# Optimization experiments

Measured on AMD Instinct MI355X. Metric: run time of the kernel, lower is better.

Reference implementation:

```python
import jax, jax.numpy as jnp
import numpy as np

HIDDEN = 1024
HEADS = 16
HEAD_DIM = HIDDEN // HEADS


def setup_inputs() -> dict:
    key = jax.random.key(0)
    kx, kq, kk, kv, ko = jax.random.split(key, 5)
    s = 1.0 / np.sqrt(HIDDEN)
    return {
        "x": jax.random.normal(kx, (2, 2048, HIDDEN), dtype=jnp.float32),
        # nn.Linear weights, stored [out, in] like torch
        "Wq": jax.random.uniform(kq, (HIDDEN, HIDDEN), jnp.float32, -s, s),
        "Wk": jax.random.uniform(kk, (HIDDEN, HIDDEN), jnp.float32, -s, s),
        "Wv": jax.random.uniform(kv, (HIDDEN, HIDDEN), jnp.float32, -s, s),
        "Wo": jax.random.uniform(ko, (HIDDEN, HIDDEN), jnp.float32, -s, s),
    }


def reference(x, Wq, Wk, Wv, Wo):
    B, S, D = x.shape
    H, Hd = HEADS, HEAD_DIM

    def proj(W):  # torch Linear: x @ W.T -> [B,H,S,Hd]
        return (x @ W.T).reshape(B, S, H, Hd).transpose(0, 2, 1, 3)

    q, k, v = proj(Wq), proj(Wk), proj(Wv)
    scores = jnp.einsum("bhsd,bhtd->bhst", q, k) / max(Hd ** 0.5, 1e-6)
    causal = jnp.tril(jnp.ones((S, S), dtype=bool))  # True = keep
    scores = jnp.where(causal, scores, -jnp.inf)
    attn = jax.nn.softmax(scores, axis=-1)
    y = jnp.einsum("bhst,bhtd->bhsd", attn, v)
    y = y.transpose(0, 2, 1, 3).reshape(B, S, D)
    return y @ Wo.T
```

## Files before the change

kernel.cpp:

```cpp
#include <hip/hip_runtime.h>
#include <hip/hip_bf16.h>


#define S_LEN  2048
#define BATCH  2
#define DMODEL 1024
#define NHEADS 16
#define HDIM   64
#define QKV_LD 3072

typedef short short8 __attribute__((ext_vector_type(8)));
typedef float f32x4  __attribute__((ext_vector_type(4)));

__device__ __forceinline__ float b2f(unsigned short u) {
    union { unsigned int i; float f; } x; x.i = ((unsigned int)u) << 16; return x.f;
}
__device__ __forceinline__ unsigned short f2b(float f) {
    union { float f; unsigned int i; } x; x.f = f;
    unsigned int r = x.i + 0x7fffu + ((x.i >> 16) & 1u);
    return (unsigned short)(r >> 16);
}

__device__ __forceinline__ void gload16(const unsigned short* g, unsigned short* l) {
    __builtin_amdgcn_global_load_lds(
        (const __attribute__((address_space(1))) unsigned int*)g,
        (__attribute__((address_space(3))) unsigned int*)l, 16, 0, 0);
}

__device__ __forceinline__ unsigned short* swzp(unsigned short* base, int row, int col) {
    int byte = (col << 1) ^ ((((row >> 3) ^ row) & 7) << 4);
    return base + (row << 6) + (byte >> 1);
}

__global__ void cast_kernel(const float* __restrict__ in, unsigned short* __restrict__ out, int n4) {
    int i = blockIdx.x * blockDim.x + threadIdx.x;
    if (i >= n4) return;
    float4 v = ((const float4*)in)[i];
    unsigned int lo = (unsigned int)f2b(v.x) | ((unsigned int)f2b(v.y) << 16);
    unsigned int hi = (unsigned int)f2b(v.z) | ((unsigned int)f2b(v.w) << 16);
    ((uint2*)out)[i] = make_uint2(lo, hi);
}

__global__ void cast_w4(const float* __restrict__ w0, const float* __restrict__ w1,
                        const float* __restrict__ w2, const float* __restrict__ w3,
                        unsigned short* __restrict__ out) {
    int i = blockIdx.x * blockDim.x + threadIdx.x;
    if (i >= (1 << 20)) return;
    int seg = i >> 18;
    const float* src = seg == 0 ? w0 : seg == 1 ? w1 : seg == 2 ? w2 : w3;
    float4 v = ((const float4*)src)[i & 0x3FFFF];
    unsigned int lo = (unsigned int)f2b(v.x) | ((unsigned int)f2b(v.y) << 16);
    unsigned int hi = (unsigned int)f2b(v.z) | ((unsigned int)f2b(v.w) << 16);
    ((uint2*)out)[i] = make_uint2(lo, hi);
}

template<int OUT_BF16>
__global__ __launch_bounds__(256) void gemm128(const unsigned short* __restrict__ A,
                                               const unsigned short* __restrict__ W,
                                               unsigned short* __restrict__ Cb,
                                               float* __restrict__ Cf,
                                               int N, int K) {
    __shared__ unsigned short As[128 * 64];
    __shared__ unsigned short Bs[128 * 64];
    const int tid  = threadIdx.x;
    const int lane = tid & 63;
    const int wave = tid >> 6;
    const int bm = blockIdx.y * 128;
    const int bn = blockIdx.x * 128;
    const int wr = (wave >> 1) * 64;
    const int wc = (wave & 1) * 64;
    const int l15 = lane & 15;
    const int l4  = lane >> 4;

    const int srow = wave * 32 + (lane >> 3);
    const int scol = (lane & 7) * 8;
    const unsigned short* Ag = A + (size_t)(bm + srow) * K + scol;
    const unsigned short* Wg = W + (size_t)(bn + srow) * K + scol;
    unsigned short* Al = As + wave * 32 * 64;
    unsigned short* Bl = Bs + wave * 32 * 64;

    f32x4 acc[4][4];
#pragma unroll
    for (int i = 0; i < 4; ++i)
#pragma unroll
        for (int j = 0; j < 4; ++j) acc[i][j] = (f32x4){0.f, 0.f, 0.f, 0.f};

    for (int k0 = 0; k0 < K; k0 += 64) {
        __syncthreads();
#pragma unroll
        for (int i = 0; i < 4; ++i) {
            gload16(Ag + k0 + (size_t)(i * 8) * K, Al + i * 8 * 64);
            gload16(Wg + k0 + (size_t)(i * 8) * K, Bl + i * 8 * 64);
        }
        __syncthreads();
#pragma unroll
        for (int kk = 0; kk < 2; ++kk) {
            short8 af[4], bf[4];
#pragma unroll
            for (int mi = 0; mi < 4; ++mi)
                af[mi] = *(const short8*)&As[(wr + mi * 16 + l15) * 64 + kk * 32 + l4 * 8];
#pragma unroll
            for (int ni = 0; ni < 4; ++ni)
                bf[ni] = *(const short8*)&Bs[(wc + ni * 16 + l15) * 64 + kk * 32 + l4 * 8];
#pragma unroll
            for (int mi = 0; mi < 4; ++mi)
#pragma unroll
                for (int ni = 0; ni < 4; ++ni)
                    acc[mi][ni] = __builtin_amdgcn_mfma_f32_16x16x32_bf16(af[mi], bf[ni], acc[mi][ni], 0, 0, 0);
        }
    }
#pragma unroll
    for (int mi = 0; mi < 4; ++mi)
#pragma unroll
        for (int ni = 0; ni < 4; ++ni)
#pragma unroll
            for (int i = 0; i < 4; ++i) {
                int row = bm + wr + mi * 16 + l4 * 4 + i;
                int col = bn + wc + ni * 16 + l15;
                float v = acc[mi][ni][i];
                if constexpr (OUT_BF16) Cb[(size_t)row * N + col] = f2b(v);
                else                    Cf[(size_t)row * N + col] = v;
            }
}

__global__ __launch_bounds__(256) void attn_mfma(const unsigned short* __restrict__ Qp,
                                                 const unsigned short* __restrict__ Kp,
                                                 const unsigned short* __restrict__ Vp,
                                                 unsigned short* __restrict__ Yp) {
    __shared__ unsigned short Ks[64 * 64];
    __shared__ unsigned short Vt[64 * 64];
    __shared__ unsigned short Pl[4 * 16 * 64];
    const int tid  = threadIdx.x;
    const int lane = tid & 63;
    const int wq   = tid >> 6;
    const int l15  = lane & 15;
    const int l4   = lane >> 4;
    const int r    = tid >> 2;
    const int c4   = tid & 3;
    const int h = blockIdx.y, b = blockIdx.z;
    unsigned short* Pw = Pl + wq * (16 * 64);

#pragma unroll 1
    for (int qp = 0; qp < 2; ++qp) {
        const int qt = qp ? (31 - (int)blockIdx.x) : (int)blockIdx.x;
        short8 qf0, qf1;
        {
            const unsigned short* qb = Qp + ((size_t)(b * S_LEN + qt * 64 + wq * 16 + l15)) * QKV_LD
                                          + h * HDIM + l4 * 8;
            qf0 = *(const short8*)qb;
            qf1 = *(const short8*)(qb + 32);
        }
        f32x4 oacc[4];
        float mrow[4], lrow[4];
#pragma unroll
        for (int t = 0; t < 4; ++t) oacc[t] = (f32x4){0.f, 0.f, 0.f, 0.f};
#pragma unroll
        for (int i = 0; i < 4; ++i) { mrow[i] = -1e30f; lrow[i] = 0.f; }

#pragma unroll 1
        for (int kt = 0; kt <= qt; ++kt) {
            __syncthreads();
            {
                const size_t gb = ((size_t)(b * S_LEN + kt * 64 + r)) * QKV_LD + h * HDIM + c4 * 16;
                uint4 k0 = *(const uint4*)(Kp + gb);
                uint4 k1 = *(const uint4*)(Kp + gb + 8);
                uint4 v0 = *(const uint4*)(Vp + gb);
                uint4 v1 = *(const uint4*)(Vp + gb + 8);
                *(uint4*)swzp(Ks, r, c4 * 16)     = k0;
                *(uint4*)swzp(Ks, r, c4 * 16 + 8) = k1;
                const unsigned short* vs = (const unsigned short*)&v0;
#pragma unroll
                for (int j = 0; j < 8; ++j) *swzp(Vt, c4 * 16 + j, r) = vs[j];
                vs = (const unsigned short*)&v1;
#pragma unroll
                for (int j = 0; j < 8; ++j) *swzp(Vt, c4 * 16 + 8 + j, r) = vs[j];
            }
            __syncthreads();

            f32x4 sc[4];
#pragma unroll
            for (int t = 0; t < 4; ++t) sc[t] = (f32x4){0.f, 0.f, 0.f, 0.f};
#pragma unroll
            for (int t = 0; t < 4; ++t) {
                short8 kf = *(const short8*)swzp(Ks, t * 16 + l15, l4 * 8);
                sc[t] = __builtin_amdgcn_mfma_f32_16x16x32_bf16(qf0, kf, sc[t], 0, 0, 0);
            }
#pragma unroll
            for (int t = 0; t < 4; ++t) {
                short8 kf = *(const short8*)swzp(Ks, t * 16 + l15, 32 + l4 * 8);
                sc[t] = __builtin_amdgcn_mfma_f32_16x16x32_bf16(qf1, kf, sc[t], 0, 0, 0);
            }
            const bool diag = (kt == qt);
#pragma unroll
            for (int t = 0; t < 4; ++t)
#pragma unroll
                for (int i = 0; i < 4; ++i) {
                    float s = sc[t][i] * 0.125f;
                    if (diag && (t * 16 + l15 > wq * 16 + l4 * 4 + i)) s = -1e30f;
                    sc[t][i] = s;
                }
#pragma unroll
            for (int i = 0; i < 4; ++i) {
                float mx = fmaxf(fmaxf(sc[0][i], sc[1][i]), fmaxf(sc[2][i], sc[3][i]));
                mx = fmaxf(mx, __shfl_xor(mx, 1));
                mx = fmaxf(mx, __shfl_xor(mx, 2));
                mx = fmaxf(mx, __shfl_xor(mx, 4));
                mx = fmaxf(mx, __shfl_xor(mx, 8));
                const float mn = fmaxf(mrow[i], mx);
                const float al = __expf(mrow[i] - mn);
                mrow[i] = mn;
                float ls = 0.f;
#pragma unroll
                for (int t = 0; t < 4; ++t) {
                    float p = __expf(sc[t][i] - mn);
                    sc[t][i] = p;
                    ls += p;
                }
                ls += __shfl_xor(ls, 1);
                ls += __shfl_xor(ls, 2);
                ls += __shfl_xor(ls, 4);
                ls += __shfl_xor(ls, 8);
                lrow[i] = lrow[i] * al + ls;
#pragma unroll
                for (int t = 0; t < 4; ++t) oacc[t][i] *= al;
            }
#pragma unroll
            for (int t = 0; t < 4; ++t)
#pragma unroll
                for (int i = 0; i < 4; ++i)
                    *swzp(Pw, l4 * 4 + i, t * 16 + l15) = f2b(sc[t][i]);

            short8 pf0 = *(const short8*)swzp(Pw, l15, l4 * 8);
            short8 pf1 = *(const short8*)swzp(Pw, l15, 32 + l4 * 8);
#pragma unroll
            for (int td = 0; td < 4; ++td) {
                short8 vf = *(const short8*)swzp(Vt, td * 16 + l15, l4 * 8);
                oacc[td] = __builtin_amdgcn_mfma_f32_16x16x32_bf16(pf0, vf, oacc[td], 0, 0, 0);
            }
#pragma unroll
            for (int td = 0; td < 4; ++td) {
                short8 vf = *(const short8*)swzp(Vt, td * 16 + l15, 32 + l4 * 8);
                oacc[td] = __builtin_amdgcn_mfma_f32_16x16x32_bf16(pf1, vf, oacc[td], 0, 0, 0);
            }
        }
        float linv[4];
#pragma unroll
        for (int i = 0; i < 4; ++i) linv[i] = 1.0f / lrow[i];
        unsigned short* yb = Yp + ((size_t)(b * S_LEN + qt * 64 + wq * 16 + l4 * 4)) * DMODEL
                                + h * HDIM + l15;
#pragma unroll
        for (int i = 0; i < 4; ++i)
#pragma unroll
            for (int td = 0; td < 4; ++td)
                yb[(size_t)i * DMODEL + td * 16] = f2b(oacc[td][i] * linv[i]);
    }
}

extern "C" void kernel_launch(void* const* d_in, const int* in_sizes, int n_in,
                              void* d_out, int out_size, void* d_ws, size_t ws_size,
                              hipStream_t stream) {
    (void)in_sizes; (void)n_in; (void)out_size; (void)ws_size;
    const float* x  = (const float*)d_in[0];
    const float* Wq = (const float*)d_in[1];
    const float* Wk = (const float*)d_in[2];
    const float* Wv = (const float*)d_in[3];
    const float* Wo = (const float*)d_in[4];
    float* out = (float*)d_out;

    const size_t nx = (size_t)BATCH * S_LEN * DMODEL;
    const size_t nw = (size_t)DMODEL * DMODEL;
    char* ws = (char*)d_ws;
    unsigned short* xb    = (unsigned short*)ws; ws += nx * 2;
    unsigned short* wqkvb = (unsigned short*)ws; ws += nw * 3 * 2;
    unsigned short* wob   = (unsigned short*)ws; ws += nw * 2;
    unsigned short* qkv   = (unsigned short*)ws; ws += nx * 3 * 2;
    unsigned short* yb    = (unsigned short*)ws; ws += nx * 2;

    cast_kernel<<<(int)(nx / 4 + 255) / 256, 256, 0, stream>>>(x, xb, (int)(nx / 4));
    cast_w4<<<(1 << 20) / 256, 256, 0, stream>>>(Wq, Wk, Wv, Wo, wqkvb);

    dim3 gq(QKV_LD / 128, (BATCH * S_LEN) / 128);
    gemm128<1><<<gq, 256, 0, stream>>>(xb, wqkvb, qkv, nullptr, QKV_LD, DMODEL);

    dim3 ga(S_LEN / 128, NHEADS, BATCH);
    attn_mfma<<<ga, 256, 0, stream>>>(qkv, qkv + DMODEL, qkv + 2 * DMODEL, yb);

    dim3 go(DMODEL / 128, (BATCH * S_LEN) / 128);
    gemm128<0><<<go, 256, 0, stream>>>(yb, wob, nullptr, out, DMODEL, DMODEL);
}
```

Measured before the change: 241.2 us.

## Double-buffer K/V tiles with register prefetch and fold softmax scale into QKV GEMM

The attention loop now stages K/V tiles through two LDS buffers and prefetches the next tile's global loads into registers while the current tile is computed. This leaves one barrier per iteration instead of two and hides global load latency. The 1/sqrt(d) scale moves into the QKV projection epilogue, applied to the Q columns before the bf16 store, so the per-score multiply disappears. The cost is doubled K/V shared memory and extra live registers, which may reduce occupancy, plus a slight change in where bf16 rounding happens.

```diff
diff --git a/kernel.cpp b/kernel.cpp
--- a/kernel.cpp
+++ b/kernel.cpp
@@ -118,8 +118,12 @@
                 int row = bm + wr + mi * 16 + l4 * 4 + i;
                 int col = bn + wc + ni * 16 + l15;
                 float v = acc[mi][ni][i];
-                if constexpr (OUT_BF16) Cb[(size_t)row * N + col] = f2b(v);
-                else                    Cf[(size_t)row * N + col] = v;
+                if constexpr (OUT_BF16) {
+                    if (col < DMODEL) v *= 0.125f;
+                    Cb[(size_t)row * N + col] = f2b(v);
+                } else {
+                    Cf[(size_t)row * N + col] = v;
+                }
             }
 }
 
@@ -127,8 +131,8 @@
                                                  const unsigned short* __restrict__ Kp,
                                                  const unsigned short* __restrict__ Vp,
                                                  unsigned short* __restrict__ Yp) {
-    __shared__ unsigned short Ks[64 * 64];
-    __shared__ unsigned short Vt[64 * 64];
+    __shared__ unsigned short Ks[2][64 * 64];
+    __shared__ unsigned short Vt[2][64 * 64];
     __shared__ unsigned short Pl[4 * 16 * 64];
     const int tid  = threadIdx.x;
     const int lane = tid & 63;
@@ -157,37 +161,51 @@
 #pragma unroll
         for (int i = 0; i < 4; ++i) { mrow[i] = -1e30f; lrow[i] = 0.f; }
 
+        uint4 rk0, rk1, rv0, rv1;
+        {
+            const size_t gb = ((size_t)(b * S_LEN + r)) * QKV_LD + h * HDIM + c4 * 16;
+            rk0 = *(const uint4*)(Kp + gb);
+            rk1 = *(const uint4*)(Kp + gb + 8);
+            rv0 = *(const uint4*)(Vp + gb);
+            rv1 = *(const uint4*)(Vp + gb + 8);
+        }
+
 #pragma unroll 1
         for (int kt = 0; kt <= qt; ++kt) {
+            const int cur = kt & 1;
+            unsigned short* Kc = (unsigned short*)Ks[cur];
+            unsigned short* Vc = (unsigned short*)Vt[cur];
+            *(uint4*)swzp(Kc, r, c4 * 16)     = rk0;
+            *(uint4*)swzp(Kc, r, c4 * 16 + 8) = rk1;
+            {
+                const unsigned short* vs = (const unsigned short*)&rv0;
+#pragma unroll
+                for (int j = 0; j < 8; ++j) *swzp(Vc, c4 * 16 + j, r) = vs[j];
+                vs = (const unsigned short*)&rv1;
+#pragma unroll
+                for (int j = 0; j < 8; ++j) *swzp(Vc, c4 * 16 + 8 + j, r) = vs[j];
+            }
+            if (kt < qt) {
+                const size_t gb = ((size_t)(b * S_LEN + (kt + 1) * 64 + r)) * QKV_LD
+                                  + h * HDIM + c4 * 16;
+                rk0 = *(const uint4*)(Kp + gb);
+                rk1 = *(const uint4*)(Kp + gb + 8);
+                rv0 = *(const uint4*)(Vp + gb);
+                rv1 = *(const uint4*)(Vp + gb + 8);
+            }
             __syncthreads();
-            {
-                const size_t gb = ((size_t)(b * S_LEN + kt * 64 + r)) * QKV_LD + h * HDIM + c4 * 16;
-                uint4 k0 = *(const uint4*)(Kp + gb);
-                uint4 k1 = *(const uint4*)(Kp + gb + 8);
-                uint4 v0 = *(const uint4*)(Vp + gb);
-                uint4 v1 = *(const uint4*)(Vp + gb + 8);
-                *(uint4*)swzp(Ks, r, c4 * 16)     = k0;
-                *(uint4*)swzp(Ks, r, c4 * 16 + 8) = k1;
-                const unsigned short* vs = (const unsigned short*)&v0;
-#pragma unroll
-                for (int j = 0; j < 8; ++j) *swzp(Vt, c4 * 16 + j, r) = vs[j];
-                vs = (const unsigned short*)&v1;
-#pragma unroll
-                for (int j = 0; j < 8; ++j) *swzp(Vt, c4 * 16 + 8 + j, r) = vs[j];
-            }
-            __syncthreads();
 
             f32x4 sc[4];
 #pragma unroll
             for (int t = 0; t < 4; ++t) sc[t] = (f32x4){0.f, 0.f, 0.f, 0.f};
 #pragma unroll
             for (int t = 0; t < 4; ++t) {
-                short8 kf = *(const short8*)swzp(Ks, t * 16 + l15, l4 * 8);
+                short8 kf = *(const short8*)swzp(Kc, t * 16 + l15, l4 * 8);
                 sc[t] = __builtin_amdgcn_mfma_f32_16x16x32_bf16(qf0, kf, sc[t], 0, 0, 0);
             }
 #pragma unroll
             for (int t = 0; t < 4; ++t) {
-                short8 kf = *(const short8*)swzp(Ks, t * 16 + l15, 32 + l4 * 8);
+                short8 kf = *(const short8*)swzp(Kc, t * 16 + l15, 32 + l4 * 8);
                 sc[t] = __builtin_amdgcn_mfma_f32_16x16x32_bf16(qf1, kf, sc[t], 0, 0, 0);
             }
             const bool diag = (kt == qt);
@@ -195,7 +213,7 @@
             for (int t = 0; t < 4; ++t)
 #pragma unroll
                 for (int i = 0; i < 4; ++i) {
-                    float s = sc[t][i] * 0.125f;
+                    float s = sc[t][i];
                     if (diag && (t * 16 + l15 > wq * 16 + l4 * 4 + i)) s = -1e30f;
                     sc[t][i] = s;
                 }
@@ -234,15 +252,17 @@
             short8 pf1 = *(const short8*)swzp(Pw, l15, 32 + l4 * 8);
 #pragma unroll
             for (int td = 0; td < 4; ++td) {
-                short8 vf = *(const short8*)swzp(Vt, td * 16 + l15, l4 * 8);
+                short8 vf = *(const short8*)swzp(Vc, td * 16 + l15, l4 * 8);
                 oacc[td] = __builtin_amdgcn_mfma_f32_16x16x32_bf16(pf0, vf, oacc[td], 0, 0, 0);
             }
 #pragma unroll
             for (int td = 0; td < 4; ++td) {
-                short8 vf = *(const short8*)swzp(Vt, td * 16 + l15, 32 + l4 * 8);
+                short8 vf = *(const short8*)swzp(Vc, td * 16 + l15, 32 + l4 * 8);
                 oacc[td] = __builtin_amdgcn_mfma_f32_16x16x32_bf16(pf1, vf, oacc[td], 0, 0, 0);
             }
         }
+        __syncthreads();
+
         float linv[4];
 #pragma unroll
         for (int i = 0; i < 4; ++i) linv[i] = 1.0f / lrow[i];
```

Measured after the change: 231.3 us. 1.04x faster.

## Widen attention key tiles to 128, fold softmax scale into Q, merge cast kernels

Applied to the files above, without the earlier changes.

The attention kernel now processes 128 keys per iteration instead of 64, which halves the number of barrier-separated loads and online-softmax rescales per query tile. LDS use grows for K, V-transposed and P. The 1/sqrt(d) scale moves into the QKV GEMM epilogue, applied to the Q columns before the bf16 store, so the per-score multiply in the attention loop goes away. The two cast kernels are merged into one launch. The risks are more masked wasted work on the diagonal block, higher register and LDS pressure lowering occupancy, and a slight change in rounding because Q is scaled before bf16 conversion.

```diff
diff --git a/kernel.cpp b/kernel.cpp
--- a/kernel.cpp
+++ b/kernel.cpp
@@ -27,31 +27,35 @@
         (__attribute__((address_space(3))) unsigned int*)l, 16, 0, 0);
 }
 
-__device__ __forceinline__ unsigned short* swzp(unsigned short* base, int row, int col) {
+__device__ __forceinline__ unsigned short* swz64(unsigned short* base, int row, int col) {
     int byte = (col << 1) ^ ((((row >> 3) ^ row) & 7) << 4);
     return base + (row << 6) + (byte >> 1);
 }
-
-__global__ void cast_kernel(const float* __restrict__ in, unsigned short* __restrict__ out, int n4) {
+__device__ __forceinline__ unsigned short* swz128(unsigned short* base, int row, int col) {
+    int byte = (col << 1) ^ ((((row >> 3) ^ row) & 7) << 4);
+    return base + (row << 7) + (byte >> 1);
+}
+
+__global__ void cast_all(const float* __restrict__ x,
+                         const float* __restrict__ w0, const float* __restrict__ w1,
+                         const float* __restrict__ w2, const float* __restrict__ w3,
+                         unsigned short* __restrict__ xb, unsigned short* __restrict__ wout) {
     int i = blockIdx.x * blockDim.x + threadIdx.x;
-    if (i >= n4) return;
-    float4 v = ((const float4*)in)[i];
+    float4 v;
+    unsigned short* dst;
+    if (i < (1 << 20)) {
+        v = ((const float4*)x)[i];
+        dst = xb + (size_t)i * 4;
+    } else {
+        int j = i - (1 << 20);
+        int seg = j >> 18;
+        const float* src = seg == 0 ? w0 : seg == 1 ? w1 : seg == 2 ? w2 : w3;
+        v = ((const float4*)src)[j & 0x3FFFF];
+        dst = wout + (size_t)j * 4;
+    }
     unsigned int lo = (unsigned int)f2b(v.x) | ((unsigned int)f2b(v.y) << 16);
     unsigned int hi = (unsigned int)f2b(v.z) | ((unsigned int)f2b(v.w) << 16);
-    ((uint2*)out)[i] = make_uint2(lo, hi);
-}
-
-__global__ void cast_w4(const float* __restrict__ w0, const float* __restrict__ w1,
-                        const float* __restrict__ w2, const float* __restrict__ w3,
-                        unsigned short* __restrict__ out) {
-    int i = blockIdx.x * blockDim.x + threadIdx.x;
-    if (i >= (1 << 20)) return;
-    int seg = i >> 18;
-    const float* src = seg == 0 ? w0 : seg == 1 ? w1 : seg == 2 ? w2 : w3;
-    float4 v = ((const float4*)src)[i & 0x3FFFF];
-    unsigned int lo = (unsigned int)f2b(v.x) | ((unsigned int)f2b(v.y) << 16);
-    unsigned int hi = (unsigned int)f2b(v.z) | ((unsigned int)f2b(v.w) << 16);
-    ((uint2*)out)[i] = make_uint2(lo, hi);
+    *(uint2*)dst = make_uint2(lo, hi);
 }
 
 template<int OUT_BF16>
@@ -118,8 +122,12 @@
                 int row = bm + wr + mi * 16 + l4 * 4 + i;
                 int col = bn + wc + ni * 16 + l15;
                 float v = acc[mi][ni][i];
-                if constexpr (OUT_BF16) Cb[(size_t)row * N + col] = f2b(v);
-                else                    Cf[(size_t)row * N + col] = v;
+                if constexpr (OUT_BF16) {
+                    if (col < DMODEL) v *= 0.125f;
+                    Cb[(size_t)row * N + col] = f2b(v);
+                } else {
+                    Cf[(size_t)row * N + col] = v;
+                }
             }
 }
 
@@ -127,18 +135,18 @@
                                                  const unsigned short* __restrict__ Kp,
                                                  const unsigned short* __restrict__ Vp,
                                                  unsigned short* __restrict__ Yp) {
-    __shared__ unsigned short Ks[64 * 64];
-    __shared__ unsigned short Vt[64 * 64];
-    __shared__ unsigned short Pl[4 * 16 * 64];
+    __shared__ unsigned short Ks[128 * 64];
+    __shared__ unsigned short Vt[64 * 128];
+    __shared__ unsigned short Pl[4 * 16 * 128];
     const int tid  = threadIdx.x;
     const int lane = tid & 63;
     const int wq   = tid >> 6;
     const int l15  = lane & 15;
     const int l4   = lane >> 4;
-    const int r    = tid >> 2;
-    const int c4   = tid & 3;
+    const int rk   = tid >> 1;
+    const int ck   = (tid & 1) * 32;
     const int h = blockIdx.y, b = blockIdx.z;
-    unsigned short* Pw = Pl + wq * (16 * 64);
+    unsigned short* Pw = Pl + wq * (16 * 128);
 
 #pragma unroll 1
     for (int qp = 0; qp < 2; ++qp) {
@@ -157,51 +165,68 @@
 #pragma unroll
         for (int i = 0; i < 4; ++i) { mrow[i] = -1e30f; lrow[i] = 0.f; }
 
+        const int nk = qt / 2 + 1;
 #pragma unroll 1
-        for (int kt = 0; kt <= qt; ++kt) {
+        for (int kb = 0; kb < nk; ++kb) {
             __syncthreads();
             {
-                const size_t gb = ((size_t)(b * S_LEN + kt * 64 + r)) * QKV_LD + h * HDIM + c4 * 16;
+                const size_t gb = ((size_t)(b * S_LEN + kb * 128 + rk)) * QKV_LD + h * HDIM + ck;
                 uint4 k0 = *(const uint4*)(Kp + gb);
                 uint4 k1 = *(const uint4*)(Kp + gb + 8);
+                uint4 k2 = *(const uint4*)(Kp + gb + 16);
+                uint4 k3 = *(const uint4*)(Kp + gb + 24);
                 uint4 v0 = *(const uint4*)(Vp + gb);
                 uint4 v1 = *(const uint4*)(Vp + gb + 8);
-                *(uint4*)swzp(Ks, r, c4 * 16)     = k0;
-                *(uint4*)swzp(Ks, r, c4 * 16 + 8) = k1;
-                const unsigned short* vs = (const unsigned short*)&v0;
-#pragma unroll
-                for (int j = 0; j < 8; ++j) *swzp(Vt, c4 * 16 + j, r) = vs[j];
+                uint4 v2 = *(const uint4*)(Vp + gb + 16);
+                uint4 v3 = *(const uint4*)(Vp + gb + 24);
+                *(uint4*)swz64(Ks, rk, ck)      = k0;
+                *(uint4*)swz64(Ks, rk, ck + 8)  = k1;
+                *(uint4*)swz64(Ks, rk, ck + 16) = k2;
+                *(uint4*)swz64(Ks, rk, ck + 24) = k3;
+                const unsigned short* vs;
+                vs = (const unsigned short*)&v0;
+#pragma unroll
+                for (int j = 0; j < 8; ++j) *swz128(Vt, ck + j, rk) = vs[j];
                 vs = (const unsigned short*)&v1;
 #pragma unroll
-                for (int j = 0; j < 8; ++j) *swzp(Vt, c4 * 16 + 8 + j, r) = vs[j];
+                for (int j = 0; j < 8; ++j) *swz128(Vt, ck + 8 + j, rk) = vs[j];
+                vs = (const unsigned short*)&v2;
+#pragma unroll
+                for (int j = 0; j < 8; ++j) *swz128(Vt, ck + 16 + j, rk) = vs[j];
+                vs = (const unsigned short*)&v3;
+#pragma unroll
+                for (int j = 0; j < 8; ++j) *swz128(Vt, ck + 24 + j, rk) = vs[j];
             }
             __syncthreads();
 
-            f32x4 sc[4];
-#pragma unroll
-            for (int t = 0; t < 4; ++t) sc[t] = (f32x4){0.f, 0.f, 0.f, 0.f};
-#pragma unroll
-            for (int t = 0; t < 4; ++t) {
-                short8 kf = *(const short8*)swzp(Ks, t * 16 + l15, l4 * 8);
+            f32x4 sc[8];
+#pragma unroll
+            for (int t = 0; t < 8; ++t) sc[t] = (f32x4){0.f, 0.f, 0.f, 0.f};
+#pragma unroll
+            for (int t = 0; t < 8; ++t) {
+                short8 kf = *(const short8*)swz64(Ks, t * 16 + l15, l4 * 8);
                 sc[t] = __builtin_amdgcn_mfma_f32_16x16x32_bf16(qf0, kf, sc[t], 0, 0, 0);
             }
 #pragma unroll
-            for (int t = 0; t < 4; ++t) {
-                short8 kf = *(const short8*)swzp(Ks, t * 16 + l15, 32 + l4 * 8);
+            for (int t = 0; t < 8; ++t) {
+                short8 kf = *(const short8*)swz64(Ks, t * 16 + l15, 32 + l4 * 8);
                 sc[t] = __builtin_amdgcn_mfma_f32_16x16x32_bf16(qf1, kf, sc[t], 0, 0, 0);
             }
-            const bool diag = (kt == qt);
-#pragma unroll
-            for (int t = 0; t < 4; ++t)
-#pragma unroll
-                for (int i = 0; i < 4; ++i) {
-                    float s = sc[t][i] * 0.125f;
-                    if (diag && (t * 16 + l15 > wq * 16 + l4 * 4 + i)) s = -1e30f;
-                    sc[t][i] = s;
-                }
+            if (kb == nk - 1) {
+#pragma unroll
+                for (int t = 0; t < 8; ++t)
+#pragma unroll
+                    for (int i = 0; i < 4; ++i) {
+                        const int key = kb * 128 + t * 16 + l15;
+                        const int qg  = qt * 64 + wq * 16 + l4 * 4 + i;
+                        if (key > qg) sc[t][i] = -1e30f;
+                    }
+            }
 #pragma unroll
             for (int i = 0; i < 4; ++i) {
-                float mx = fmaxf(fmaxf(sc[0][i], sc[1][i]), fmaxf(sc[2][i], sc[3][i]));
+                float mx = sc[0][i];
+#pragma unroll
+                for (int t = 1; t < 8; ++t) mx = fmaxf(mx, sc[t][i]);
                 mx = fmaxf(mx, __shfl_xor(mx, 1));
                 mx = fmaxf(mx, __shfl_xor(mx, 2));
                 mx = fmaxf(mx, __shfl_xor(mx, 4));
@@ -211,7 +236,7 @@
                 mrow[i] = mn;
                 float ls = 0.f;
 #pragma unroll
-                for (int t = 0; t < 4; ++t) {
+                for (int t = 0; t < 8; ++t) {
                     float p = __expf(sc[t][i] - mn);
                     sc[t][i] = p;
                     ls += p;
@@ -222,25 +247,22 @@
                 ls += __shfl_xor(ls, 8);
                 lrow[i] = lrow[i] * al + ls;
 #pragma unroll
-                for (int t = 0; t < 4; ++t) oacc[t][i] *= al;
-            }
-#pragma unroll
-            for (int t = 0; t < 4; ++t)
+                for (int td = 0; td < 4; ++td) oacc[td][i] *= al;
+            }
+#pragma unroll
+            for (int t = 0; t < 8; ++t)
 #pragma unroll
                 for (int i = 0; i < 4; ++i)
-                    *swzp(Pw, l4 * 4 + i, t * 16 + l15) = f2b(sc[t][i]);
-
-            short8 pf0 = *(const short8*)swzp(Pw, l15, l4 * 8);
-            short8 pf1 = *(const short8*)swzp(Pw, l15, 32 + l4 * 8);
-#pragma unroll
-            for (int td = 0; td < 4; ++td) {
-                short8 vf = *(const short8*)swzp(Vt, td * 16 + l15, l4 * 8);
-                oacc[td] = __builtin_amdgcn_mfma_f32_16x16x32_bf16(pf0, vf, oacc[td], 0, 0, 0);
-            }
-#pragma unroll
-            for (int td = 0; td < 4; ++td) {
-                short8 vf = *(const short8*)swzp(Vt, td * 16 + l15, 32 + l4 * 8);
-                oacc[td] = __builtin_amdgcn_mfma_f32_16x16x32_bf16(pf1, vf, oacc[td], 0, 0, 0);
+                    *swz128(Pw, l4 * 4 + i, t * 16 + l15) = f2b(sc[t][i]);
+
+#pragma unroll
+            for (int ks = 0; ks < 4; ++ks) {
+                short8 pf = *(const short8*)swz128(Pw, l15, ks * 32 + l4 * 8);
+#pragma unroll
+                for (int td = 0; td < 4; ++td) {
+                    short8 vf = *(const short8*)swz128(Vt, td * 16 + l15, ks * 32 + l4 * 8);
+                    oacc[td] = __builtin_amdgcn_mfma_f32_16x16x32_bf16(pf, vf, oacc[td], 0, 0, 0);
+                }
             }
         }
         float linv[4];
@@ -276,8 +298,7 @@
     unsigned short* qkv   = (unsigned short*)ws; ws += nx * 3 * 2;
     unsigned short* yb    = (unsigned short*)ws; ws += nx * 2;
 
-    cast_kernel<<<(int)(nx / 4 + 255) / 256, 256, 0, stream>>>(x, xb, (int)(nx / 4));
-    cast_w4<<<(1 << 20) / 256, 256, 0, stream>>>(Wq, Wk, Wv, Wo, wqkvb);
+    cast_all<<<(1 << 21) / 256, 256, 0, stream>>>(x, Wq, Wk, Wv, Wo, xb, wqkvb);
 
     dim3 gq(QKV_LD / 128, (BATCH * S_LEN) / 128);
     gemm128<1><<<gq, 256, 0, stream>>>(xb, wqkvb, qkv, nullptr, QKV_LD, DMODEL);
```

After: 224.3 us. -7.0%, faster.
